# Kernel optimization log

Hardware: AMD Instinct MI355X
Metric: run time of the kernel (lower is better)

## Reference

```python
import jax, jax.numpy as jnp
import numpy as np

EMBED_DIM = 1024
NUM_HEADS = 16
HEAD_DIM = EMBED_DIM // NUM_HEADS
B, S = 4, 2048


def setup_inputs() -> dict:
    key = jax.random.key(0)
    ks = jax.random.split(key, 9)
    s = 1.0 / np.sqrt(EMBED_DIM)
    x = jax.random.normal(ks[0], (B, S, EMBED_DIM), dtype=jnp.float32)
    # nn.Linear weights stored [out, in]; y = x @ W.T + b
    Wq = jax.random.uniform(ks[1], (EMBED_DIM, EMBED_DIM), jnp.float32, -s, s)
    bq = jax.random.uniform(ks[2], (EMBED_DIM,), jnp.float32, -s, s)
    Wk = jax.random.uniform(ks[3], (EMBED_DIM, EMBED_DIM), jnp.float32, -s, s)
    bk = jax.random.uniform(ks[4], (EMBED_DIM,), jnp.float32, -s, s)
    Wv = jax.random.uniform(ks[5], (EMBED_DIM, EMBED_DIM), jnp.float32, -s, s)
    bv = jax.random.uniform(ks[6], (EMBED_DIM,), jnp.float32, -s, s)
    Wo = jax.random.uniform(ks[7], (EMBED_DIM, EMBED_DIM), jnp.float32, -s, s)
    bo = jax.random.uniform(ks[8], (EMBED_DIM,), jnp.float32, -s, s)
    return {"x": x, "Wq": Wq, "bq": bq, "Wk": Wk, "bk": bk,
            "Wv": Wv, "bv": bv, "Wo": Wo, "bo": bo}


def _split_heads(t):
    b, s, _ = t.shape
    return t.reshape(b, s, NUM_HEADS, HEAD_DIM).transpose(0, 2, 1, 3)  # [B,H,S,D]


def reference(x, Wq, bq, Wk, bk, Wv, bv, Wo, bo):
    q = _split_heads(x @ Wq.T + bq)
    k = _split_heads(x @ Wk.T + bk)
    v = _split_heads(x @ Wv.T + bv)
    scores = jnp.einsum('bhqd,bhkd->bhqk', q, k) / np.sqrt(HEAD_DIM)  # [B,H,S,S]
    attn = jax.nn.softmax(scores, axis=-1)
    ctx = jnp.einsum('bhqk,bhkd->bhqd', attn, v)          # [B,H,S,D]
    ctx = ctx.transpose(0, 2, 1, 3).reshape(x.shape[0], x.shape[1], EMBED_DIM)
    return ctx @ Wo.T + bo
```

## Files before the change

### kernel.cpp

```cpp
#include <hip/hip_runtime.h>
#include <hip/hip_bf16.h>
#include <stdint.h>

typedef __attribute__((ext_vector_type(8))) short  bf16x8;
typedef __attribute__((ext_vector_type(4))) float  f32x4;

#define LOG2E 1.4426950408889634f

__device__ __forceinline__ unsigned short f2bf(float f) {
  unsigned int u = __builtin_bit_cast(unsigned int, f);
  u += 0x7fffu + ((u >> 16) & 1u);
  return (unsigned short)(u >> 16);
}

__device__ __forceinline__ unsigned int pk2(float a, float b) {
  __hip_bfloat162 h = __float22bfloat162_rn(make_float2(a, b));
  unsigned int u;
  __builtin_memcpy(&u, &h, 4);
  return u;
}

__device__ __forceinline__ void async16(const void* g, void* l) {
  __builtin_amdgcn_global_load_lds(
      (const __attribute__((address_space(1))) unsigned int*)g,
      (__attribute__((address_space(3))) unsigned int*)l,
      16, 0, 0);
}

__global__ __launch_bounds__(256) void cast_all(
    const float* __restrict__ x,
    const float* __restrict__ Wq, const float* __restrict__ Wk,
    const float* __restrict__ Wv, const float* __restrict__ Wo,
    unsigned short* __restrict__ xb, unsigned short* __restrict__ wqkv,
    unsigned short* __restrict__ wo) {
  int i = blockIdx.x * 256 + threadIdx.x;
  const float* src;
  unsigned short* dst;
  int off;
  if (i < 2097152) {
    src = x; dst = xb; off = i;
  } else {
    int j = i - 2097152;
    int seg = j >> 18; off = j & 262143;
    src = (seg == 0) ? Wq : (seg == 1) ? Wk : (seg == 2) ? Wv : Wo;
    dst = (seg < 3) ? (wqkv + (size_t)seg * 1048576) : wo;
  }
  float4 f = ((const float4*)src)[off];
  uint2 o;
  o.x = pk2(f.x, f.y);
  o.y = pk2(f.z, f.w);
  ((uint2*)dst)[off] = o;
}

__global__ __launch_bounds__(256) void gemm_qkv(
    const unsigned short* __restrict__ xb, const unsigned short* __restrict__ wqkv,
    const float* __restrict__ bq, const float* __restrict__ bk, const float* __restrict__ bv,
    unsigned short* __restrict__ qb, unsigned short* __restrict__ kb,
    unsigned short* __restrict__ vb) {
  __shared__ __align__(16) unsigned short As[128 * 32];
  __shared__ __align__(16) unsigned short Bs[128 * 32];
  __shared__ __align__(16) unsigned short epi[4][64 * 72];
  const int bid = blockIdx.x;
  const int xcd = bid & 7, idx = bid >> 3;
  const int nt = xcd * 3 + (idx % 3);
  const int mt = idx / 3;
  const int m0 = mt * 128, n0 = nt * 128;
  const int tid = threadIdx.x;
  const int wv = tid >> 6, lane = tid & 63, qq = lane >> 4, ln = lane & 15;
  const int wm = wv & 1, wn = wv >> 1;
  const int K = 1024;

  f32x4 acc[4][4];
#pragma unroll
  for (int i = 0; i < 4; ++i)
#pragma unroll
    for (int j = 0; j < 4; ++j) acc[i][j] = f32x4{0.f, 0.f, 0.f, 0.f};

  for (int k0 = 0; k0 < K; k0 += 32) {
#pragma unroll
    for (int i = 0; i < 2; ++i) {
      int cc = wv * 2 + i;
      int jp = cc * 64 + lane;
      int row = jp >> 2, cp = jp & 3;
      int c = cp ^ ((row >> 1) & 3);
      async16(xb   + (size_t)(m0 + row) * K + k0 + c * 8, As + cc * 512);
      async16(wqkv + (size_t)(n0 + row) * K + k0 + c * 8, Bs + cc * 512);
    }
    __syncthreads();
    bf16x8 af[4], bf[4];
#pragma unroll
    for (int i = 0; i < 4; ++i) {
      int row = wm * 64 + i * 16 + ln;
      af[i] = *(const bf16x8*)(As + row * 32 + (qq ^ ((row >> 1) & 3)) * 8);
    }
#pragma unroll
    for (int j = 0; j < 4; ++j) {
      int row = wn * 64 + j * 16 + ln;
      bf[j] = *(const bf16x8*)(Bs + row * 32 + (qq ^ ((row >> 1) & 3)) * 8);
    }
#pragma unroll
    for (int i = 0; i < 4; ++i)
#pragma unroll
      for (int j = 0; j < 4; ++j)
        acc[i][j] = __builtin_amdgcn_mfma_f32_16x16x32_bf16(af[i], bf[j], acc[i][j], 0, 0, 0);
    __syncthreads();
  }

  const int nblk = n0 >> 10;
  const float* bias = (nblk == 0) ? bq : (nblk == 1) ? bk : bv;
  const float scale = (nblk == 0) ? (0.125f * LOG2E) : 1.0f;
  unsigned short* buf = epi[wv];
  const int ncol0 = (n0 & 1023) + wn * 64;
  const int head  = ncol0 >> 6;
  const int mbase = m0 + wm * 64;
  const int b     = mbase >> 11, sbase = mbase & 2047;
  unsigned short* dst = (nblk == 0) ? qb : (nblk == 1) ? kb : vb;

  if (nblk != 2) {
#pragma unroll
    for (int j = 0; j < 4; ++j) {
      float bs = bias[ncol0 + j * 16 + ln] * scale;
#pragma unroll
      for (int i = 0; i < 4; ++i)
#pragma unroll
        for (int r = 0; r < 4; ++r)
          buf[(i * 16 + qq * 4 + r) * 72 + j * 16 + ln] = f2bf(acc[i][j][r] * scale + bs);
    }
    unsigned short* gout = dst + (((size_t)(b * 16 + head)) * 2048 + sbase) * 64;
#pragma unroll
    for (int h = 0; h < 2; ++h)
#pragma unroll
      for (int p = 0; p < 4; ++p) {
        int rr = (lane >> 2) + p * 16;
        int c4 = lane & 3;
        ulonglong2 v = *(const ulonglong2*)(buf + rr * 72 + h * 32 + c4 * 8);
        *(ulonglong2*)(gout + (size_t)rr * 64 + h * 32 + c4 * 8) = v;
      }
  } else {
#pragma unroll
    for (int j = 0; j < 4; ++j) {
      float bs = bias[ncol0 + j * 16 + ln];
#pragma unroll
      for (int i = 0; i < 4; ++i) {
        uint2 pk;
        pk.x = pk2(acc[i][j][0] + bs, acc[i][j][1] + bs);
        pk.y = pk2(acc[i][j][2] + bs, acc[i][j][3] + bs);
        *(uint2*)(buf + (j * 16 + ln) * 72 + i * 16 + qq * 4) = pk;
      }
    }
    unsigned short* gout = dst + ((size_t)(b * 16 + head)) * 64 * 2048 + sbase;
#pragma unroll
    for (int p = 0; p < 8; ++p) {
      int dr = (lane >> 3) + p * 8;
      int c8 = lane & 7;
      ulonglong2 v = *(const ulonglong2*)(buf + dr * 72 + c8 * 8);
      *(ulonglong2*)(gout + (size_t)dr * 2048 + c8 * 8) = v;
    }
  }
}

__global__ __launch_bounds__(256, 4) void attn_kernel(
    const unsigned short* __restrict__ qb, const unsigned short* __restrict__ kb,
    const unsigned short* __restrict__ vb, unsigned short* __restrict__ ctx) {
  __shared__ __align__(16) unsigned short k_sh[64 * 64];
  __shared__ __align__(16) unsigned short vT_sh[64 * 64];
  __shared__ __align__(16) unsigned short p_sh[128 * 72];
  const int bid = blockIdx.x;
  const int xcd = bid & 7, idx = bid >> 3;
  const int bh = xcd * 8 + (idx >> 4);
  const int q0 = (idx & 15) * 128;
  const int tid = threadIdx.x;
  const int wv = tid >> 6, lane = tid & 63, qq = lane >> 4, ln = lane & 15;

  bf16x8 qf[2][2];
  {
    const unsigned short* qbase = qb + ((size_t)bh * 2048 + q0 + wv * 32) * 64;
#pragma unroll
    for (int rb = 0; rb < 2; ++rb)
#pragma unroll
      for (int kq = 0; kq < 2; ++kq)
        qf[rb][kq] = *(const bf16x8*)(qbase + (rb * 16 + ln) * 64 + kq * 32 + qq * 8);
  }

  f32x4 o_acc[2][4];
  float l_i[2] = {0.f, 0.f};
#pragma unroll
  for (int rb = 0; rb < 2; ++rb)
#pragma unroll
    for (int nt = 0; nt < 4; ++nt) o_acc[rb][nt] = f32x4{0.f, 0.f, 0.f, 0.f};

  const unsigned short* kgbase = kb + (size_t)bh * 2048 * 64;
  const unsigned short* vgbase = vb + (size_t)bh * 64 * 2048;

  for (int kt = 0; kt < 32; ++kt) {
#pragma unroll
    for (int i = 0; i < 2; ++i) {
      int cc = wv * 2 + i;
      int jp = cc * 64 + lane;
      int row = jp >> 3, cp = jp & 7;
      int c = cp ^ (row & 7);
      async16(kgbase + (size_t)(kt * 64 + row) * 64 + c * 8, k_sh + cc * 512);
      async16(vgbase + (size_t)row * 2048 + kt * 64 + c * 8, vT_sh + cc * 512);
    }
    __syncthreads();

    f32x4 s_acc[2][4];
#pragma unroll
    for (int rb = 0; rb < 2; ++rb)
#pragma unroll
      for (int ct = 0; ct < 4; ++ct) s_acc[rb][ct] = f32x4{0.f, 0.f, 0.f, 0.f};
#pragma unroll
    for (int ct = 0; ct < 4; ++ct) {
      int row = ct * 16 + ln;
      bf16x8 kf0 = *(const bf16x8*)(k_sh + row * 64 + ((0 + qq) ^ (row & 7)) * 8);
      bf16x8 kf1 = *(const bf16x8*)(k_sh + row * 64 + ((4 + qq) ^ (row & 7)) * 8);
#pragma unroll
      for (int rb = 0; rb < 2; ++rb) {
        s_acc[rb][ct] = __builtin_amdgcn_mfma_f32_16x16x32_bf16(kf0, qf[rb][0], s_acc[rb][ct], 0, 0, 0);
        s_acc[rb][ct] = __builtin_amdgcn_mfma_f32_16x16x32_bf16(kf1, qf[rb][1], s_acc[rb][ct], 0, 0, 0);
      }
    }

#pragma unroll
    for (int rb = 0; rb < 2; ++rb) {
      int prow = wv * 32 + rb * 16 + ln;
      float sum = 0.f;
#pragma unroll
      for (int ct = 0; ct < 4; ++ct) {
        float p0 = __builtin_amdgcn_exp2f(s_acc[rb][ct][0]);
        float p1 = __builtin_amdgcn_exp2f(s_acc[rb][ct][1]);
        float p2 = __builtin_amdgcn_exp2f(s_acc[rb][ct][2]);
        float p3 = __builtin_amdgcn_exp2f(s_acc[rb][ct][3]);
        sum += (p0 + p1) + (p2 + p3);
        uint2 pk;
        pk.x = pk2(p0, p1);
        pk.y = pk2(p2, p3);
        *(uint2*)(p_sh + prow * 72 + ct * 16 + qq * 4) = pk;
      }
      l_i[rb] += sum;
    }

#pragma unroll
    for (int kk = 0; kk < 2; ++kk) {
      bf16x8 vf[4], pf[2];
#pragma unroll
      for (int nt = 0; nt < 4; ++nt) {
        int row = nt * 16 + ln;
        vf[nt] = *(const bf16x8*)(vT_sh + row * 64 + ((kk * 4 + qq) ^ (row & 7)) * 8);
      }
#pragma unroll
      for (int rb = 0; rb < 2; ++rb) {
        int row = wv * 32 + rb * 16 + ln;
        pf[rb] = *(const bf16x8*)(p_sh + row * 72 + kk * 32 + qq * 8);
      }
#pragma unroll
      for (int rb = 0; rb < 2; ++rb)
#pragma unroll
        for (int nt = 0; nt < 4; ++nt)
          o_acc[rb][nt] = __builtin_amdgcn_mfma_f32_16x16x32_bf16(vf[nt], pf[rb], o_acc[rb][nt], 0, 0, 0);
    }
    __syncthreads();
  }

#pragma unroll
  for (int rb = 0; rb < 2; ++rb) {
    l_i[rb] += __shfl_xor(l_i[rb], 16);
    l_i[rb] += __shfl_xor(l_i[rb], 32);
    float inv = 1.0f / l_i[rb];
    int row = wv * 32 + rb * 16 + ln;
#pragma unroll
    for (int nt = 0; nt < 4; ++nt) {
      uint2 pk;
      pk.x = pk2(o_acc[rb][nt][0] * inv, o_acc[rb][nt][1] * inv);
      pk.y = pk2(o_acc[rb][nt][2] * inv, o_acc[rb][nt][3] * inv);
      *(uint2*)(p_sh + row * 72 + nt * 16 + qq * 4) = pk;
    }
  }
  __syncthreads();
  {
    const int b = bh >> 4, h = bh & 15;
    int r = tid >> 1, half = tid & 1;
    int s = q0 + r;
    size_t gbase = ((size_t)(b * 2048 + s)) * 1024 + h * 64 + half * 32;
    const unsigned short* lsrc = p_sh + r * 72 + half * 32;
#pragma unroll
    for (int j = 0; j < 4; ++j)
      ((ulonglong2*)(ctx + gbase + j * 8))[0] = ((const ulonglong2*)(lsrc + j * 8))[0];
  }
}

__global__ __launch_bounds__(256) void gemm_out(
    const unsigned short* __restrict__ ctx, const unsigned short* __restrict__ wo,
    const float* __restrict__ bo, float* __restrict__ out) {
  __shared__ __align__(16) unsigned short As[128 * 32];
  __shared__ __align__(16) unsigned short Bs[128 * 32];
  const int bid = blockIdx.x;
  const int n0 = (bid & 7) * 128;
  const int m0 = (bid >> 3) * 128;
  const int tid = threadIdx.x;
  const int wv = tid >> 6, lane = tid & 63, qq = lane >> 4, ln = lane & 15;
  const int wm = wv & 1, wn = wv >> 1;
  const int K = 1024;

  f32x4 acc[4][4];
#pragma unroll
  for (int i = 0; i < 4; ++i)
#pragma unroll
    for (int j = 0; j < 4; ++j) acc[i][j] = f32x4{0.f, 0.f, 0.f, 0.f};

  for (int k0 = 0; k0 < K; k0 += 32) {
#pragma unroll
    for (int i = 0; i < 2; ++i) {
      int cc = wv * 2 + i;
      int jp = cc * 64 + lane;
      int row = jp >> 2, cp = jp & 3;
      int c = cp ^ ((row >> 1) & 3);
      async16(ctx + (size_t)(m0 + row) * K + k0 + c * 8, As + cc * 512);
      async16(wo  + (size_t)(n0 + row) * K + k0 + c * 8, Bs + cc * 512);
    }
    __syncthreads();
    bf16x8 af[4], bf[4];
#pragma unroll
    for (int i = 0; i < 4; ++i) {
      int row = wm * 64 + i * 16 + ln;
      af[i] = *(const bf16x8*)(As + row * 32 + (qq ^ ((row >> 1) & 3)) * 8);
    }
#pragma unroll
    for (int j = 0; j < 4; ++j) {
      int row = wn * 64 + j * 16 + ln;
      bf[j] = *(const bf16x8*)(Bs + row * 32 + (qq ^ ((row >> 1) & 3)) * 8);
    }
#pragma unroll
    for (int i = 0; i < 4; ++i)
#pragma unroll
      for (int j = 0; j < 4; ++j)
        acc[i][j] = __builtin_amdgcn_mfma_f32_16x16x32_bf16(af[i], bf[j], acc[i][j], 0, 0, 0);
    __syncthreads();
  }

#pragma unroll
  for (int j = 0; j < 4; ++j) {
    int n = n0 + wn * 64 + j * 16 + ln;
    float bsv = bo[n];
#pragma unroll
    for (int i = 0; i < 4; ++i) {
#pragma unroll
      for (int r = 0; r < 4; ++r) {
        int m = m0 + wm * 64 + i * 16 + qq * 4 + r;
        out[(size_t)m * 1024 + n] = acc[i][j][r] + bsv;
      }
    }
  }
}

extern "C" void kernel_launch(void* const* d_in, const int* in_sizes, int n_in,
                              void* d_out, int out_size, void* d_ws, size_t ws_size,
                              hipStream_t stream) {
  const float* x  = (const float*)d_in[0];
  const float* Wq = (const float*)d_in[1];
  const float* bq = (const float*)d_in[2];
  const float* Wk = (const float*)d_in[3];
  const float* bk = (const float*)d_in[4];
  const float* Wv = (const float*)d_in[5];
  const float* bv = (const float*)d_in[6];
  const float* Wo = (const float*)d_in[7];
  const float* bo = (const float*)d_in[8];
  float* out = (float*)d_out;

  char* ws = (char*)d_ws;
  unsigned short* xb   = (unsigned short*)(ws);
  unsigned short* ctxb = (unsigned short*)(ws);
  unsigned short* qb   = (unsigned short*)(ws + ((size_t)16 << 20));
  unsigned short* kbuf = (unsigned short*)(ws + ((size_t)32 << 20));
  unsigned short* vbuf = (unsigned short*)(ws + ((size_t)48 << 20));
  unsigned short* wqkv = (unsigned short*)(ws + ((size_t)64 << 20));
  unsigned short* wo   = (unsigned short*)(ws + ((size_t)70 << 20));

  cast_all<<<12288, 256, 0, stream>>>(x, Wq, Wk, Wv, Wo, xb, wqkv, wo);

  gemm_qkv<<<1536, 256, 0, stream>>>(xb, wqkv, bq, bk, bv, qb, kbuf, vbuf);
  attn_kernel<<<1024, 256, 0, stream>>>(qb, kbuf, vbuf, ctxb);
  gemm_out<<<512, 256, 0, stream>>>(ctxb, wo, bo, out);
}
```

Measured before the change: 281.8 us.

## Double-buffer K tiles and GEMM operands with async prefetch and split waits

The attention kernel now double-buffers K in shared memory, prefetches the next K tile before computing, and loads the next V tile after the PV MMA, using explicit vmcnt waits and raw barriers in place of full syncthreads. The P buffer switches from padded rows to an XOR-swizzled 64-wide layout, which saves LDS. MFMA sections are wrapped in setprio. The output GEMM also gets double-buffered A/B tiles with prefetch. The goal is to hide global-load latency behind MFMA work, at the cost of fragile manual waitcnt accounting and more LDS in the GEMM.

```diff
diff --git a/kernel.cpp b/kernel.cpp
--- a/kernel.cpp
+++ b/kernel.cpp
@@ -162,9 +162,9 @@
 __global__ __launch_bounds__(256, 4) void attn_kernel(
     const unsigned short* __restrict__ qb, const unsigned short* __restrict__ kb,
     const unsigned short* __restrict__ vb, unsigned short* __restrict__ ctx) {
-  __shared__ __align__(16) unsigned short k_sh[64 * 64];
+  __shared__ __align__(16) unsigned short k_sh[2][64 * 64];
   __shared__ __align__(16) unsigned short vT_sh[64 * 64];
-  __shared__ __align__(16) unsigned short p_sh[128 * 72];
+  __shared__ __align__(16) unsigned short p_sh[128 * 64];
   const int bid = blockIdx.x;
   const int xcd = bid & 7, idx = bid >> 3;
   const int bh = xcd * 8 + (idx >> 4);
@@ -191,39 +191,61 @@
 
   const unsigned short* kgbase = kb + (size_t)bh * 2048 * 64;
   const unsigned short* vgbase = vb + (size_t)bh * 64 * 2048;
+  const int cc0 = wv * 2;
+
+  auto stageK = [&](int kt, unsigned short* dst) {
+#pragma unroll
+    for (int i = 0; i < 2; ++i) {
+      int jp = (cc0 + i) * 64 + lane;
+      int row = jp >> 3, c = (jp & 7) ^ (row & 7);
+      async16(kgbase + (size_t)(kt * 64 + row) * 64 + c * 8, dst + (cc0 + i) * 512);
+    }
+  };
+  auto stageV = [&](int kt) {
+#pragma unroll
+    for (int i = 0; i < 2; ++i) {
+      int jp = (cc0 + i) * 64 + lane;
+      int row = jp >> 3, c = (jp & 7) ^ (row & 7);
+      async16(vgbase + (size_t)row * 2048 + kt * 64 + c * 8, vT_sh + (cc0 + i) * 512);
+    }
+  };
+
+  stageK(0, k_sh[0]);
+  stageV(0);
 
   for (int kt = 0; kt < 32; ++kt) {
-#pragma unroll
-    for (int i = 0; i < 2; ++i) {
-      int cc = wv * 2 + i;
-      int jp = cc * 64 + lane;
-      int row = jp >> 3, cp = jp & 7;
-      int c = cp ^ (row & 7);
-      async16(kgbase + (size_t)(kt * 64 + row) * 64 + c * 8, k_sh + cc * 512);
-      async16(vgbase + (size_t)row * 2048 + kt * 64 + c * 8, vT_sh + cc * 512);
-    }
-    __syncthreads();
+    const unsigned short* kcur = k_sh[kt & 1];
+    if (kt < 31) {
+      stageK(kt + 1, k_sh[(kt & 1) ^ 1]);
+      asm volatile("s_waitcnt vmcnt(4)" ::: "memory");
+    } else {
+      asm volatile("s_waitcnt vmcnt(2)" ::: "memory");
+    }
+    __builtin_amdgcn_s_barrier();
 
     f32x4 s_acc[2][4];
 #pragma unroll
     for (int rb = 0; rb < 2; ++rb)
 #pragma unroll
       for (int ct = 0; ct < 4; ++ct) s_acc[rb][ct] = f32x4{0.f, 0.f, 0.f, 0.f};
+    __builtin_amdgcn_s_setprio(1);
 #pragma unroll
     for (int ct = 0; ct < 4; ++ct) {
       int row = ct * 16 + ln;
-      bf16x8 kf0 = *(const bf16x8*)(k_sh + row * 64 + ((0 + qq) ^ (row & 7)) * 8);
-      bf16x8 kf1 = *(const bf16x8*)(k_sh + row * 64 + ((4 + qq) ^ (row & 7)) * 8);
+      bf16x8 kf0 = *(const bf16x8*)(kcur + row * 64 + ((0 + qq) ^ (row & 7)) * 8);
+      bf16x8 kf1 = *(const bf16x8*)(kcur + row * 64 + ((4 + qq) ^ (row & 7)) * 8);
 #pragma unroll
       for (int rb = 0; rb < 2; ++rb) {
         s_acc[rb][ct] = __builtin_amdgcn_mfma_f32_16x16x32_bf16(kf0, qf[rb][0], s_acc[rb][ct], 0, 0, 0);
         s_acc[rb][ct] = __builtin_amdgcn_mfma_f32_16x16x32_bf16(kf1, qf[rb][1], s_acc[rb][ct], 0, 0, 0);
       }
     }
+    __builtin_amdgcn_s_setprio(0);
 
 #pragma unroll
     for (int rb = 0; rb < 2; ++rb) {
       int prow = wv * 32 + rb * 16 + ln;
+      int rs = prow & 7;
       float sum = 0.f;
 #pragma unroll
       for (int ct = 0; ct < 4; ++ct) {
@@ -235,10 +257,14 @@
         uint2 pk;
         pk.x = pk2(p0, p1);
         pk.y = pk2(p2, p3);
-        *(uint2*)(p_sh + prow * 72 + ct * 16 + qq * 4) = pk;
+        *(uint2*)(p_sh + prow * 64 + (((ct * 2 + (qq >> 1)) ^ rs) << 3) + ((qq & 1) << 2)) = pk;
       }
       l_i[rb] += sum;
     }
+
+    if (kt < 31) asm volatile("s_waitcnt vmcnt(2)" ::: "memory");
+    else         asm volatile("s_waitcnt vmcnt(0)" ::: "memory");
+    __builtin_amdgcn_s_barrier();
 
 #pragma unroll
     for (int kk = 0; kk < 2; ++kk) {
@@ -251,15 +277,18 @@
 #pragma unroll
       for (int rb = 0; rb < 2; ++rb) {
         int row = wv * 32 + rb * 16 + ln;
-        pf[rb] = *(const bf16x8*)(p_sh + row * 72 + kk * 32 + qq * 8);
-      }
+        pf[rb] = *(const bf16x8*)(p_sh + row * 64 + (((kk * 4 + qq) ^ (row & 7)) << 3));
+      }
+      __builtin_amdgcn_s_setprio(1);
 #pragma unroll
       for (int rb = 0; rb < 2; ++rb)
 #pragma unroll
         for (int nt = 0; nt < 4; ++nt)
           o_acc[rb][nt] = __builtin_amdgcn_mfma_f32_16x16x32_bf16(vf[nt], pf[rb], o_acc[rb][nt], 0, 0, 0);
-    }
-    __syncthreads();
+      __builtin_amdgcn_s_setprio(0);
+    }
+    __builtin_amdgcn_s_barrier();
+    if (kt < 31) stageV(kt + 1);
   }
 
 #pragma unroll
@@ -268,32 +297,34 @@
     l_i[rb] += __shfl_xor(l_i[rb], 32);
     float inv = 1.0f / l_i[rb];
     int row = wv * 32 + rb * 16 + ln;
+    int rs = row & 7;
 #pragma unroll
     for (int nt = 0; nt < 4; ++nt) {
       uint2 pk;
       pk.x = pk2(o_acc[rb][nt][0] * inv, o_acc[rb][nt][1] * inv);
       pk.y = pk2(o_acc[rb][nt][2] * inv, o_acc[rb][nt][3] * inv);
-      *(uint2*)(p_sh + row * 72 + nt * 16 + qq * 4) = pk;
-    }
-  }
-  __syncthreads();
+      *(uint2*)(p_sh + row * 64 + (((nt * 2 + (qq >> 1)) ^ rs) << 3) + ((qq & 1) << 2)) = pk;
+    }
+  }
   {
     const int b = bh >> 4, h = bh & 15;
     int r = tid >> 1, half = tid & 1;
+    int rs = r & 7;
     int s = q0 + r;
     size_t gbase = ((size_t)(b * 2048 + s)) * 1024 + h * 64 + half * 32;
-    const unsigned short* lsrc = p_sh + r * 72 + half * 32;
+    const unsigned short* lsrc = p_sh + r * 64;
 #pragma unroll
     for (int j = 0; j < 4; ++j)
-      ((ulonglong2*)(ctx + gbase + j * 8))[0] = ((const ulonglong2*)(lsrc + j * 8))[0];
+      ((ulonglong2*)(ctx + gbase + j * 8))[0] =
+          *(const ulonglong2*)(lsrc + (((half * 4 + j) ^ rs) << 3));
   }
 }
 
 __global__ __launch_bounds__(256) void gemm_out(
     const unsigned short* __restrict__ ctx, const unsigned short* __restrict__ wo,
     const float* __restrict__ bo, float* __restrict__ out) {
-  __shared__ __align__(16) unsigned short As[128 * 32];
-  __shared__ __align__(16) unsigned short Bs[128 * 32];
+  __shared__ __align__(16) unsigned short As[2][128 * 32];
+  __shared__ __align__(16) unsigned short Bs[2][128 * 32];
   const int bid = blockIdx.x;
   const int n0 = (bid & 7) * 128;
   const int m0 = (bid >> 3) * 128;
@@ -308,34 +339,46 @@
 #pragma unroll
     for (int j = 0; j < 4; ++j) acc[i][j] = f32x4{0.f, 0.f, 0.f, 0.f};
 
-  for (int k0 = 0; k0 < K; k0 += 32) {
+  auto stage = [&](int t, int buf) {
 #pragma unroll
     for (int i = 0; i < 2; ++i) {
       int cc = wv * 2 + i;
       int jp = cc * 64 + lane;
       int row = jp >> 2, cp = jp & 3;
       int c = cp ^ ((row >> 1) & 3);
-      async16(ctx + (size_t)(m0 + row) * K + k0 + c * 8, As + cc * 512);
-      async16(wo  + (size_t)(n0 + row) * K + k0 + c * 8, Bs + cc * 512);
-    }
-    __syncthreads();
+      async16(ctx + (size_t)(m0 + row) * K + t * 32 + c * 8, As[buf] + cc * 512);
+      async16(wo  + (size_t)(n0 + row) * K + t * 32 + c * 8, Bs[buf] + cc * 512);
+    }
+  };
+
+  stage(0, 0);
+  for (int t = 0; t < 32; ++t) {
+    const int cur = t & 1;
+    if (t < 31) {
+      stage(t + 1, cur ^ 1);
+      asm volatile("s_waitcnt vmcnt(4)" ::: "memory");
+    } else {
+      asm volatile("s_waitcnt vmcnt(0)" ::: "memory");
+    }
+    __builtin_amdgcn_s_barrier();
+
     bf16x8 af[4], bf[4];
 #pragma unroll
     for (int i = 0; i < 4; ++i) {
       int row = wm * 64 + i * 16 + ln;
-      af[i] = *(const bf16x8*)(As + row * 32 + (qq ^ ((row >> 1) & 3)) * 8);
+      af[i] = *(const bf16x8*)(As[cur] + row * 32 + (qq ^ ((row >> 1) & 3)) * 8);
     }
 #pragma unroll
     for (int j = 0; j < 4; ++j) {
       int row = wn * 64 + j * 16 + ln;
-      bf[j] = *(const bf16x8*)(Bs + row * 32 + (qq ^ ((row >> 1) & 3)) * 8);
+      bf[j] = *(const bf16x8*)(Bs[cur] + row * 32 + (qq ^ ((row >> 1) & 3)) * 8);
     }
 #pragma unroll
     for (int i = 0; i < 4; ++i)
 #pragma unroll
       for (int j = 0; j < 4; ++j)
         acc[i][j] = __builtin_amdgcn_mfma_f32_16x16x32_bf16(af[i], bf[j], acc[i][j], 0, 0, 0);
-    __syncthreads();
+    __builtin_amdgcn_s_barrier();
   }
 
 #pragma unroll
```

Result: no change. 283.9 us (+0.7%).
